# Kernel tuning notes

Measured on AMD Instinct MI355X. Metric: run time of the kernel, lower is better.

## Reference

```python
import jax, jax.numpy as jnp
import numpy as np

S = 2048      # seq len (q and kv)
D_MODEL = 2048
H = 16        # num heads
HD = D_MODEL // H  # head dim = 128


def softmax1(x):
    # off-by-one softmax: denominator has extra exp(-m) term (the '1' = e^0 shifted by max)
    m = jnp.maximum(jax.lax.stop_gradient(x.max(-1, keepdims=True)), 0)
    un = jnp.exp(x - m)
    return un / (jnp.exp(-m) + jnp.sum(un, axis=-1, keepdims=True))


def setup_inputs() -> dict:
    key = jax.random.key(0)
    ks = jax.random.split(key, 8)
    std = 1.0 / np.sqrt(D_MODEL)
    return {
        "query": jax.random.normal(ks[0], (S, D_MODEL), jnp.float32),
        "key_": jax.random.normal(ks[1], (S, D_MODEL), jnp.float32),
        "value": jax.random.normal(ks[2], (S, D_MODEL), jnp.float32),
        "Wq": jax.random.uniform(ks[3], (D_MODEL, D_MODEL), jnp.float32, -std, std),
        "Wk": jax.random.uniform(ks[4], (D_MODEL, D_MODEL), jnp.float32, -std, std),
        "Wv": jax.random.uniform(ks[5], (D_MODEL, D_MODEL), jnp.float32, -std, std),
        "Wo": jax.random.uniform(ks[6], (D_MODEL, D_MODEL), jnp.float32, -std, std),
        "scalars": jnp.ones((H,), jnp.float32),
    }


def reference(query, key_, value, Wq, Wk, Wv, Wo, scalars):
    # equinox Linear: y = W @ x, weight shape (out, in), no bias
    qh = (query @ Wq.T).reshape(S, H, HD)   # [S, H, HD]
    kh = (key_ @ Wk.T).reshape(S, H, HD)
    vh = (value @ Wv.T).reshape(S, H, HD)
    scale = 1.0 / jnp.sqrt(jnp.asarray(HD, qh.dtype))
    logits = jnp.einsum("qhd,khd->hqk", qh * scale, kh)  # [H, S, S]
    w = softmax1(logits)
    attn = jnp.einsum("hqk,khd->qhd", w, vh)             # [S, H, HD]
    attn = attn * scalars[None, :, None]
    return attn.reshape(S, H * HD) @ Wo.T                # [S, D_MODEL]
```

## Files before the change

kernel.cpp:

```cpp
#include <hip/hip_runtime.h>
#include <hip/hip_bf16.h>


#define S_LEN 2048
#define DMODEL 2048
#define NHEAD 16
#define HEADD 128

typedef __bf16 bf16x8 __attribute__((ext_vector_type(8)));
typedef __bf16 bf16x4 __attribute__((ext_vector_type(4)));
typedef float f32x4 __attribute__((ext_vector_type(4)));

__device__ inline void async_copy16(const __bf16* g, __bf16* l) {
    __builtin_amdgcn_global_load_lds(
        (const __attribute__((address_space(1))) unsigned int*)g,
        (__attribute__((address_space(3))) unsigned int*)l, 16, 0, 0);
}

__global__ __launch_bounds__(256) void conv2(const float* __restrict__ s0,
                                             __hip_bfloat16* __restrict__ h0,
                                             __hip_bfloat16* __restrict__ l0,
                                             float sc0,
                                             const float* __restrict__ s1,
                                             __hip_bfloat16* __restrict__ h1,
                                             __hip_bfloat16* __restrict__ l1,
                                             float sc1) {
    const float* s = blockIdx.y ? s1 : s0;
    __hip_bfloat16* ph = blockIdx.y ? h1 : h0;
    __hip_bfloat16* pl = blockIdx.y ? l1 : l0;
    const float sc = blockIdx.y ? sc1 : sc0;
    size_t i4 = (size_t)blockIdx.x * 256 + threadIdx.x;
    float4 v = *(const float4*)&s[i4 * 4];
    float x0 = v.x * sc, x1 = v.y * sc, x2 = v.z * sc, x3 = v.w * sc;
    bf16x4 hv, lv;
    __bf16 a0 = (__bf16)x0, a1 = (__bf16)x1, a2 = (__bf16)x2, a3 = (__bf16)x3;
    hv[0] = a0; hv[1] = a1; hv[2] = a2; hv[3] = a3;
    lv[0] = (__bf16)(x0 - (float)a0); lv[1] = (__bf16)(x1 - (float)a1);
    lv[2] = (__bf16)(x2 - (float)a2); lv[3] = (__bf16)(x3 - (float)a3);
    *(bf16x4*)&ph[i4 * 4] = hv;
    *(bf16x4*)&pl[i4 * 4] = lv;
}

struct GArgs {
    const __bf16 *Ah, *Al, *Bh, *Bl;
    float* Cf;
    __bf16 *Ch, *Cl;
};

template <int OUTMODE>
__global__ __launch_bounds__(256, 2) void gemm_nt3(GArgs g0, GArgs g1) {
    constexpr int K = DMODEL, N = DMODEL;
    const GArgs g = blockIdx.z ? g1 : g0;
    __shared__ __bf16 sAh[2][128 * 32], sAl[2][128 * 32];
    __shared__ __bf16 sBh[2][128 * 32], sBl[2][128 * 32];

    const int tid = threadIdx.x;
    const int lane = tid & 63;
    const int wave = tid >> 6;
    const int wr = wave >> 1;
    const int wc = wave & 1;
    const int qr = lane & 15;
    const int quad = lane >> 4;

    const int flat = blockIdx.y * gridDim.x + blockIdx.x;
    const int swz = (flat & 7) * 32 + (flat >> 3);
    const size_t row0 = (size_t)(swz >> 4) * 128;
    const size_t col0 = (size_t)(swz & 15) * 128;

    const int srow = tid >> 2;
    const int k8 = (((tid & 3) ^ ((tid >> 2) & 3)) * 8);
    const __bf16* gAh = g.Ah + (row0 + srow) * K + k8;
    const __bf16* gAl = g.Al + (row0 + srow) * K + k8;
    const __bf16* gBh = g.Bh + (col0 + srow) * K + k8;
    const __bf16* gBl = g.Bl + (col0 + srow) * K + k8;

    f32x4 acc[4][4] = {};

    auto stage = [&](int b, int k0) {
#pragma unroll
        for (int c = 0; c < 2; ++c) {
            async_copy16(gAh + k0 + (size_t)c * 64 * K, &sAh[b][c * 2048 + tid * 8]);
            async_copy16(gAl + k0 + (size_t)c * 64 * K, &sAl[b][c * 2048 + tid * 8]);
            async_copy16(gBh + k0 + (size_t)c * 64 * K, &sBh[b][c * 2048 + tid * 8]);
            async_copy16(gBl + k0 + (size_t)c * 64 * K, &sBl[b][c * 2048 + tid * 8]);
        }
    };

    stage(0, 0);
    __syncthreads();

    const int aslot = (quad ^ (qr & 3)) * 8;
    int cur = 0;
    for (int k0 = 0; k0 < K; k0 += 32) {
        if (k0 + 32 < K) stage(cur ^ 1, k0 + 32);

        bf16x8 a_h[4], a_l[4], b_h[4], b_l[4];
#pragma unroll
        for (int i = 0; i < 4; ++i) {
            a_h[i] = *(const bf16x8*)&sAh[cur][(wr * 64 + i * 16 + qr) * 32 + aslot];
            a_l[i] = *(const bf16x8*)&sAl[cur][(wr * 64 + i * 16 + qr) * 32 + aslot];
        }
#pragma unroll
        for (int j = 0; j < 4; ++j) {
            b_h[j] = *(const bf16x8*)&sBh[cur][(wc * 64 + j * 16 + qr) * 32 + aslot];
            b_l[j] = *(const bf16x8*)&sBl[cur][(wc * 64 + j * 16 + qr) * 32 + aslot];
        }
#pragma unroll
        for (int i = 0; i < 4; ++i)
#pragma unroll
            for (int j = 0; j < 4; ++j) {
                acc[i][j] = __builtin_amdgcn_mfma_f32_16x16x32_bf16(a_h[i], b_h[j], acc[i][j], 0, 0, 0);
                acc[i][j] = __builtin_amdgcn_mfma_f32_16x16x32_bf16(a_h[i], b_l[j], acc[i][j], 0, 0, 0);
                acc[i][j] = __builtin_amdgcn_mfma_f32_16x16x32_bf16(a_l[i], b_h[j], acc[i][j], 0, 0, 0);
            }
        __syncthreads();
        cur ^= 1;
    }

#pragma unroll
    for (int i = 0; i < 4; ++i)
#pragma unroll
        for (int j = 0; j < 4; ++j)
#pragma unroll
            for (int r = 0; r < 4; ++r) {
                size_t idx = (row0 + wr * 64 + i * 16 + quad * 4 + r) * N +
                             col0 + wc * 64 + j * 16 + qr;
                float x = acc[i][j][r];
                if (OUTMODE == 0) {
                    g.Cf[idx] = x;
                } else if (OUTMODE == 1) {
                    g.Ch[idx] = (__bf16)x;
                } else {
                    __bf16 hv = (__bf16)x;
                    g.Ch[idx] = hv;
                    g.Cl[idx] = (__bf16)(x - (float)hv);
                }
            }
}

__global__ __launch_bounds__(256) void attn_mfma(const __bf16* __restrict__ qhi_g,
                                                 const __bf16* __restrict__ qlo_g,
                                                 const __bf16* __restrict__ khi_g,
                                                 const __bf16* __restrict__ klo_g,
                                                 const __bf16* __restrict__ vhT,
                                                 const float* __restrict__ scalars,
                                                 __bf16* __restrict__ ohi_g,
                                                 __bf16* __restrict__ olo_g) {
    const int h = blockIdx.y;
    const int q0 = blockIdx.x * 64;
    __shared__ __align__(16) __bf16 Khi[64][136];
    __shared__ __align__(16) __bf16 Klo[64][136];
    __shared__ __align__(16) __bf16 VT[128][72];
    __shared__ __align__(16) __bf16 Ps[64][72];

    const int tid = threadIdx.x;
    const int lane = tid & 63;
    const int wave = tid >> 6;
    const int qr = lane & 15;
    const int quad = lane >> 4;

    bf16x8 qfh[4], qfl[4];
    {
        const __bf16* qrh = qhi_g + (size_t)(q0 + wave * 16 + qr) * DMODEL + h * HEADD;
        const __bf16* qrl = qlo_g + (size_t)(q0 + wave * 16 + qr) * DMODEL + h * HEADD;
#pragma unroll
        for (int kc = 0; kc < 4; ++kc) {
            qfh[kc] = *(const bf16x8*)&qrh[kc * 32 + quad * 8];
            qfl[kc] = *(const bf16x8*)&qrl[kc * 32 + quad * 8];
        }
    }

    f32x4 oacc[8] = {};
    float m_r[4], l_r[4];
#pragma unroll
    for (int r = 0; r < 4; ++r) { m_r[r] = 0.f; l_r[r] = 1.f; }

    for (int k0 = 0; k0 < S_LEN; k0 += 64) {
#pragma unroll
        for (int i = 0; i < 4; ++i) {
            int idx = tid + i * 256;
            int kp = idx >> 4;
            int c8 = (idx & 15) * 8;
            size_t goff = (size_t)(k0 + kp) * DMODEL + h * HEADD + c8;
            *(bf16x8*)&Khi[kp][c8] = *(const bf16x8*)&khi_g[goff];
            *(bf16x8*)&Klo[kp][c8] = *(const bf16x8*)&klo_g[goff];
        }
#pragma unroll
        for (int i = 0; i < 4; ++i) {
            int idx = tid + i * 256;
            int dm = idx >> 3;
            int c8 = (idx & 7) * 8;
            *(bf16x8*)&VT[dm][c8] =
                *(const bf16x8*)&vhT[(size_t)(h * HEADD + dm) * S_LEN + k0 + c8];
        }
        __syncthreads();

        f32x4 S[4] = {};
#pragma unroll
        for (int jt = 0; jt < 4; ++jt) {
#pragma unroll
            for (int kc = 0; kc < 4; ++kc) {
                bf16x8 kh8 = *(const bf16x8*)&Khi[jt * 16 + qr][kc * 32 + quad * 8];
                bf16x8 kl8 = *(const bf16x8*)&Klo[jt * 16 + qr][kc * 32 + quad * 8];
                S[jt] = __builtin_amdgcn_mfma_f32_16x16x32_bf16(qfh[kc], kh8, S[jt], 0, 0, 0);
                S[jt] = __builtin_amdgcn_mfma_f32_16x16x32_bf16(qfh[kc], kl8, S[jt], 0, 0, 0);
                S[jt] = __builtin_amdgcn_mfma_f32_16x16x32_bf16(qfl[kc], kh8, S[jt], 0, 0, 0);
            }
        }

#pragma unroll
        for (int r = 0; r < 4; ++r) {
            float mx = fmaxf(fmaxf(S[0][r], S[1][r]), fmaxf(S[2][r], S[3][r]));
#pragma unroll
            for (int m = 1; m < 16; m <<= 1) mx = fmaxf(mx, __shfl_xor(mx, m, 64));
            float m_new = fmaxf(m_r[r], mx);
            float alpha = __expf(m_r[r] - m_new);
            float sum = 0.f;
            int prow = wave * 16 + quad * 4 + r;
#pragma unroll
            for (int jt = 0; jt < 4; ++jt) {
                float e = __expf(S[jt][r] - m_new);
                sum += e;
                Ps[prow][jt * 16 + qr] = (__bf16)e;
            }
#pragma unroll
            for (int m = 1; m < 16; m <<= 1) sum += __shfl_xor(sum, m, 64);
            l_r[r] = l_r[r] * alpha + sum;
            m_r[r] = m_new;
#pragma unroll
            for (int nt = 0; nt < 8; ++nt) oacc[nt][r] *= alpha;
        }
        __syncthreads();

#pragma unroll
        for (int kc = 0; kc < 2; ++kc) {
            bf16x8 pf = *(const bf16x8*)&Ps[wave * 16 + qr][kc * 32 + quad * 8];
#pragma unroll
            for (int nt = 0; nt < 8; ++nt) {
                bf16x8 vf = *(const bf16x8*)&VT[nt * 16 + qr][kc * 32 + quad * 8];
                oacc[nt] = __builtin_amdgcn_mfma_f32_16x16x32_bf16(pf, vf, oacc[nt], 0, 0, 0);
            }
        }
        __syncthreads();
    }

    const float sh = scalars[h];
#pragma unroll
    for (int r = 0; r < 4; ++r) {
        float wm = sh / l_r[r];
        size_t rowoff = (size_t)(q0 + wave * 16 + quad * 4 + r) * DMODEL + h * HEADD;
#pragma unroll
        for (int nt = 0; nt < 8; ++nt) {
            float x = oacc[nt][r] * wm;
            __bf16 hv = (__bf16)x;
            ohi_g[rowoff + nt * 16 + qr] = hv;
            olo_g[rowoff + nt * 16 + qr] = (__bf16)(x - (float)hv);
        }
    }
}

extern "C" void kernel_launch(void* const* d_in, const int* in_sizes, int n_in,
                              void* d_out, int out_size, void* d_ws, size_t ws_size,
                              hipStream_t stream) {
    const float* query   = (const float*)d_in[0];
    const float* key_    = (const float*)d_in[1];
    const float* value   = (const float*)d_in[2];
    const float* Wq      = (const float*)d_in[3];
    const float* Wk      = (const float*)d_in[4];
    const float* Wv      = (const float*)d_in[5];
    const float* Wo      = (const float*)d_in[6];
    const float* scalars = (const float*)d_in[7];
    float* out = (float*)d_out;

    const size_t PL = (size_t)S_LEN * DMODEL;
    __bf16* p[12];
    for (int i = 0; i < 12; ++i) p[i] = (__bf16*)d_ws + i * PL;

    const float scale = 0.08838834764831844f;
    dim3 cg(2048 * 2048 / 4 / 256, 2), cb(256);
    dim3 gg(DMODEL / 128, S_LEN / 128, 1), gb(256);
    dim3 gg2(DMODEL / 128, S_LEN / 128, 2);

#define BH(x) (__hip_bfloat16*)(x)
    conv2<<<cg, cb, 0, stream>>>(query, BH(p[0]), BH(p[1]), 1.0f,
                                 Wq, BH(p[2]), BH(p[3]), scale);
    conv2<<<cg, cb, 0, stream>>>(key_, BH(p[4]), BH(p[5]), 1.0f,
                                 Wk, BH(p[6]), BH(p[7]), 1.0f);
    {
        GArgs gq = {p[0], p[1], p[2], p[3], nullptr, p[8], p[9]};
        GArgs gk = {p[4], p[5], p[6], p[7], nullptr, p[10], p[11]};
        gemm_nt3<2><<<gg2, gb, 0, stream>>>(gq, gk);
    }
    conv2<<<cg, cb, 0, stream>>>(Wv, BH(p[0]), BH(p[1]), 1.0f,
                                 value, BH(p[2]), BH(p[3]), 1.0f);
    {
        GArgs gv = {p[0], p[1], p[2], p[3], nullptr, p[4], nullptr};
        gemm_nt3<1><<<gg, gb, 0, stream>>>(gv, gv);
    }

    attn_mfma<<<dim3(S_LEN / 64, NHEAD), 256, 0, stream>>>(
        p[8], p[9], p[10], p[11], p[4], scalars, p[8], p[9]);

    conv2<<<dim3(2048 * 2048 / 4 / 256, 1), cb, 0, stream>>>(
        Wo, BH(p[0]), BH(p[1]), 1.0f, Wo, BH(p[0]), BH(p[1]), 1.0f);
    {
        GArgs go = {p[8], p[9], p[0], p[1], out, nullptr, nullptr};
        gemm_nt3<0><<<gg, gb, 0, stream>>>(go, go);
    }
#undef BH
}
```

Baseline: 541.0 us.

## Prefetch next K/V tile into registers, remap blocks by head, drop a barrier

The attention kernel now loads the next K-hi, K-lo and V^T tile from global memory into registers while the current tile is processed, then writes them to LDS at the top of the next iteration. This is meant to hide global load latency behind the MFMA and softmax work. The block index is also remapped so neighbouring blocks interleave heads and query tiles, intended to improve cache locality across the device. The barrier between softmax and the P·V step is removed, which is safe only because each wave reads back only its own Ps rows. The prefetch adds register pressure, which could lower occupancy.

New measurement: 537.3 us. Within noise of the previous version (-0.7%).

```diff
diff --git a/kernel.cpp b/kernel.cpp
--- a/kernel.cpp
+++ b/kernel.cpp
@@ -146,8 +146,11 @@
                                                  const float* __restrict__ scalars,
                                                  __bf16* __restrict__ ohi_g,
                                                  __bf16* __restrict__ olo_g) {
-    const int h = blockIdx.y;
-    const int q0 = blockIdx.x * 64;
+    const int flatb = blockIdx.y * gridDim.x + blockIdx.x;
+    const int ib = flatb >> 3;
+    const int h = (flatb & 7) * 2 + (ib >> 5);
+    const int q0 = (ib & 31) * 64;
+
     __shared__ __align__(16) __bf16 Khi[64][136];
     __shared__ __align__(16) __bf16 Klo[64][136];
     __shared__ __align__(16) __bf16 VT[128][72];
@@ -159,6 +162,14 @@
     const int qr = lane & 15;
     const int quad = lane >> 4;
 
+    const int kp0 = tid >> 4;
+    const int kc8 = (tid & 15) * 8;
+    const int dm0 = tid >> 3;
+    const int vc8 = (tid & 7) * 8;
+    const __bf16* gK_hi = khi_g + (size_t)kp0 * DMODEL + h * HEADD + kc8;
+    const __bf16* gK_lo = klo_g + (size_t)kp0 * DMODEL + h * HEADD + kc8;
+    const __bf16* gVT = vhT + (size_t)(h * HEADD + dm0) * S_LEN + vc8;
+
     bf16x8 qfh[4], qfl[4];
     {
         const __bf16* qrh = qhi_g + (size_t)(q0 + wave * 16 + qr) * DMODEL + h * HEADD;
@@ -170,30 +181,35 @@
         }
     }
 
+    bf16x8 rKh[4], rKl[4], rV[4];
+    auto load_regs = [&](int k0) {
+#pragma unroll
+        for (int i = 0; i < 4; ++i) {
+            size_t go = (size_t)(k0 + i * 16) * DMODEL;
+            rKh[i] = *(const bf16x8*)&gK_hi[go];
+            rKl[i] = *(const bf16x8*)&gK_lo[go];
+            rV[i] = *(const bf16x8*)&gVT[(size_t)(i * 32) * S_LEN + k0];
+        }
+    };
+    auto write_lds = [&]() {
+#pragma unroll
+        for (int i = 0; i < 4; ++i) {
+            *(bf16x8*)&Khi[kp0 + i * 16][kc8] = rKh[i];
+            *(bf16x8*)&Klo[kp0 + i * 16][kc8] = rKl[i];
+            *(bf16x8*)&VT[dm0 + i * 32][vc8] = rV[i];
+        }
+    };
+
     f32x4 oacc[8] = {};
     float m_r[4], l_r[4];
 #pragma unroll
     for (int r = 0; r < 4; ++r) { m_r[r] = 0.f; l_r[r] = 1.f; }
 
+    load_regs(0);
     for (int k0 = 0; k0 < S_LEN; k0 += 64) {
-#pragma unroll
-        for (int i = 0; i < 4; ++i) {
-            int idx = tid + i * 256;
-            int kp = idx >> 4;
-            int c8 = (idx & 15) * 8;
-            size_t goff = (size_t)(k0 + kp) * DMODEL + h * HEADD + c8;
-            *(bf16x8*)&Khi[kp][c8] = *(const bf16x8*)&khi_g[goff];
-            *(bf16x8*)&Klo[kp][c8] = *(const bf16x8*)&klo_g[goff];
-        }
-#pragma unroll
-        for (int i = 0; i < 4; ++i) {
-            int idx = tid + i * 256;
-            int dm = idx >> 3;
-            int c8 = (idx & 7) * 8;
-            *(bf16x8*)&VT[dm][c8] =
-                *(const bf16x8*)&vhT[(size_t)(h * HEADD + dm) * S_LEN + k0 + c8];
-        }
+        write_lds();
         __syncthreads();
+        if (k0 + 64 < S_LEN) load_regs(k0 + 64);
 
         f32x4 S[4] = {};
 #pragma unroll
@@ -230,7 +246,6 @@
 #pragma unroll
             for (int nt = 0; nt < 8; ++nt) oacc[nt][r] *= alpha;
         }
-        __syncthreads();
 
 #pragma unroll
         for (int kc = 0; kc < 2; ++kc) {
```
